# Kernel tuning notes

Hardware: AMD Instinct MI355X
Metric: run time of the kernel (lower is better)

The kernel has to match this reference:

```python
import jax, jax.numpy as jnp
import numpy as np

N_ITER = 5
B = 16            # graphs
NPG = 3125        # nodes per graph
EPG = 50000       # edges per graph
N_NODES = B * NPG # 50000
E = B * EPG       # 800000
F = 32            # f_e = f_x = f_u
H = 64            # hidden


def _lin(key, fan_in, fan_out):
    k1, k2 = jax.random.split(key)
    s = 1.0 / np.sqrt(fan_in)
    W = jax.random.uniform(k1, (fan_in, fan_out), jnp.float32, -s, s)
    b = jax.random.uniform(k2, (fan_out,), jnp.float32, -s, s)
    return W, b


def setup_inputs() -> dict:
    key = jax.random.key(0)
    ks = jax.random.split(key, 12)
    x = jax.random.normal(ks[0], (N_NODES, F), jnp.float32)
    edge_attr = jax.random.normal(ks[1], (E, F), jnp.float32)
    y = jax.random.normal(ks[2], (B, F), jnp.float32)
    # within-graph random edges: graph g owns nodes [g*NPG, (g+1)*NPG)
    off = (jnp.arange(B, dtype=jnp.int32) * NPG)[:, None]          # [B,1]
    src = jax.random.randint(ks[3], (B, EPG), 0, NPG, jnp.int32) + off
    dst = jax.random.randint(ks[4], (B, EPG), 0, NPG, jnp.int32) + off
    edge_index = jnp.stack([src.reshape(-1), dst.reshape(-1)])      # [2,E]
    batch = jnp.repeat(jnp.arange(B, dtype=jnp.int32), NPG)         # [N]
    # shared GN-block parameters (one block reused for all N_ITER steps)
    We1, be1 = _lin(ks[5], F + 2 * F + F, H)   # edge MLP: [src,dst,e,u[b]]
    We2, be2 = _lin(ks[6], H, F)
    Wn1, bn1 = _lin(ks[7], F + F + F, H)       # node MLP: [x,e_agg,u[b]]
    Wn2, bn2 = _lin(ks[8], H, F)
    Wg1, bg1 = _lin(ks[9], F + F + F, H)       # global MLP: [x_agg,e_agg,u]
    Wg2, bg2 = _lin(ks[10], H, F)
    return dict(x=x, edge_attr=edge_attr, y=y,
                We1=We1, be1=be1, We2=We2, be2=be2,
                Wn1=Wn1, bn1=bn1, Wn2=Wn2, bn2=bn2,
                Wg1=Wg1, bg1=bg1, Wg2=Wg2, bg2=bg2,
                edge_index=edge_index, batch=batch)


def _mlp(h_in, W1, b1, W2, b2):
    return jax.nn.relu(h_in @ W1 + b1) @ W2 + b2


def _segment_mean(vals, seg, num):
    s = jax.ops.segment_sum(vals, seg, num_segments=num)
    c = jax.ops.segment_sum(jnp.ones((vals.shape[0], 1), vals.dtype), seg,
                            num_segments=num)
    return s / jnp.maximum(c, 1.0)


def _gn_forward(x, edge_attr, y, params, edge_index, batch):
    (We1, be1, We2, be2, Wn1, bn1, Wn2, bn2, Wg1, bg1, Wg2, bg2) = params
    row, col = edge_index[0], edge_index[1]
    e_batch = batch[row]
    for _ in range(N_ITER):  # shared-weight unrolled GN block
        # EdgeModel: phi_e([src, dest, e, u[batch_e]])
        e_in = jnp.concatenate([x[row], x[col], edge_attr, y[e_batch]], axis=1)
        edge_attr = _mlp(e_in, We1, be1, We2, be2)
        # NodeModel: mean of incoming edges (scatter over col)
        e_agg_node = _segment_mean(edge_attr, col, N_NODES)
        n_in = jnp.concatenate([x, e_agg_node, y[batch]], axis=1)
        x = _mlp(n_in, Wn1, bn1, Wn2, bn2)
        # GlobalModel: per-graph means of edges and nodes
        e_agg = _segment_mean(edge_attr, e_batch, B)
        x_agg = _segment_mean(x, batch, B)
        g_in = jnp.concatenate([x_agg, e_agg, y], axis=1)
        y = _mlp(g_in, Wg1, bg1, Wg2, bg2)
    return x, edge_attr, y


def reference(x, edge_attr, y,
              We1, be1, We2, be2,
              Wn1, bn1, Wn2, bn2,
              Wg1, bg1, Wg2, bg2,
              edge_index, batch):
    params = (We1, be1, We2, be2, Wn1, bn1, Wn2, bn2, Wg1, bg1, Wg2, bg2)
    return _gn_forward(x, edge_attr, y, params, edge_index, batch)
```

## Files before the change

kernel.cpp:

```cpp
#include <hip/hip_runtime.h>

#define NITER   5
#define B_G     16
#define NPG     3125
#define EPG     50000
#define NNODES  50000
#define NEDGES  800000
#define FD      32
#define HD      64

#define EDGE_TPG   391
#define EDGE_BLOCKS 1024

#define NODE_TPG   25
#define NODE_BLOCKS (B_G * NODE_TPG)

typedef __attribute__((ext_vector_type(4))) float f32x4;
typedef __attribute__((ext_vector_type(8))) short bf16x8;
typedef __attribute__((ext_vector_type(4))) unsigned int u32x4;

union FragU { bf16x8 v; unsigned int u[4]; u32x4 q; };

__device__ __forceinline__ void fsplit2(float a, float b,
                                        unsigned int& hi, unsigned int& lo) {
    unsigned int ua = __float_as_uint(a), ub = __float_as_uint(b);
    float la = a - __uint_as_float(ua & 0xffff0000u);
    float lb = b - __uint_as_float(ub & 0xffff0000u);
    hi = __builtin_amdgcn_perm(ub, ua, 0x07060302u);
    lo = __builtin_amdgcn_perm(__float_as_uint(lb), __float_as_uint(la), 0x07060302u);
}
__device__ __forceinline__ unsigned int fpack_hl(float v) {
    unsigned int uv = __float_as_uint(v);
    float lv = v - __uint_as_float(uv & 0xffff0000u);
    return __builtin_amdgcn_perm(__float_as_uint(lv), uv, 0x07060302u);
}
__device__ __forceinline__ bf16x8 ldfrag(const unsigned int* p) {
    FragU t; t.q = *(const u32x4*)p; return t.v;
}

__global__ __launch_bounds__(1024) void wsplit_kernel(
    const float* __restrict__ We1, const float* __restrict__ We2,
    const float* __restrict__ Wn1, const float* __restrict__ Wn2,
    unsigned int* __restrict__ wsp)
{
    for (int item = threadIdx.x; item < 1792; item += 1024) {
        const float* W; unsigned int* dst; int lda, s, n, l;
        if (item < 768)       { int f = item >> 6;          l = item & 63; s = f >> 2; n = f & 3; W = We1; lda = 64; dst = wsp + f * 512; }
        else if (item < 1024) { int f = (item - 768) >> 6;  l = item & 63; s = f >> 1; n = f & 1; W = We2; lda = 32; dst = wsp + 6144 + f * 512; }
        else if (item < 1536) { int f = (item - 1024) >> 6; l = item & 63; s = f >> 2; n = f & 3; W = Wn1; lda = 64; dst = wsp + 8192 + f * 512; }
        else                  { int f = (item - 1536) >> 6; l = item & 63; s = f >> 1; n = f & 1; W = Wn2; lda = 32; dst = wsp + 12288 + f * 512; }
        int lm = l & 15, lg = l >> 4;
        int rowbase = s * 32 + lg * 8;
        int col = n * 16 + lm;
        #pragma unroll
        for (int p = 0; p < 4; ++p) {
            float a = W[(rowbase + 2 * p) * lda + col];
            float b = W[(rowbase + 2 * p + 1) * lda + col];
            unsigned int hi, lo;
            fsplit2(a, b, hi, lo);
            dst[l * 4 + p] = hi;
            dst[256 + l * 4 + p] = lo;
        }
    }
}


__global__ __launch_bounds__(256) void count_kernel(const int* __restrict__ coli,
                                                    int* __restrict__ cnt)
{
    int e = blockIdx.x * 256 + threadIdx.x;
    if (e < NEDGES) atomicAdd(&cnt[coli[e]], 1);
}

__global__ __launch_bounds__(1024) void scan_blocks_kernel(const int* __restrict__ deg,
                                                           int* __restrict__ off,
                                                           int* __restrict__ bsum, int n)
{
    __shared__ int buf[1024];
    int tid = threadIdx.x;
    int idx = blockIdx.x * 1024 + tid;
    int v = (idx < n) ? deg[idx] : 0;
    buf[tid] = v;
    __syncthreads();
    for (int o = 1; o < 1024; o <<= 1) {
        int t = (tid >= o) ? buf[tid - o] : 0;
        __syncthreads();
        buf[tid] += t;
        __syncthreads();
    }
    if (idx < n) off[idx] = buf[tid] - v;
    if (tid == 1023) bsum[blockIdx.x] = buf[1023];
}

__global__ __launch_bounds__(64) void scan_carry_kernel(int* __restrict__ bsum,
                                                        int* __restrict__ off,
                                                        int nb, int n)
{
    if (threadIdx.x == 0) {
        int c = 0;
        for (int i = 0; i < nb; ++i) { int t = bsum[i]; bsum[i] = c; c += t; }
        off[n] = c;
    }
}

__global__ __launch_bounds__(1024) void scan_add_kernel(const int* __restrict__ bsum,
                                                        int* __restrict__ off, int n)
{
    int idx = blockIdx.x * 1024 + threadIdx.x;
    if (idx < n) off[idx] += bsum[blockIdx.x];
}

__global__ __launch_bounds__(256) void fill_kernel(const int* __restrict__ coli,
                                                   const int* __restrict__ off,
                                                   int* __restrict__ cursor,
                                                   int* __restrict__ csr)
{
    int e = blockIdx.x * 256 + threadIdx.x;
    if (e < NEDGES) {
        int c = coli[e];
        int pos = atomicAdd(&cursor[c], 1);
        csr[off[c] + pos] = e;
    }
}


__global__ __launch_bounds__(1024) void prep_kernel(
    const float* __restrict__ y,
    const float* __restrict__ We1, const float* __restrict__ be1,
    const float* __restrict__ Wn1, const float* __restrict__ bn1,
    float* __restrict__ cu_e, float* __restrict__ cu_n,
    float* __restrict__ xagg, float* __restrict__ eagg)
{
    int tid = threadIdx.x;
    if (tid < B_G * FD) xagg[tid] = 0.0f;
    else                eagg[tid - B_G * FD] = 0.0f;

    int g = tid >> 6;
    int j = tid & 63;
    float ae = be1[j];
    float an = bn1[j];
    for (int k = 0; k < FD; ++k) {
        float yv = y[g * FD + k];
        ae = fmaf(yv, We1[(96 + k) * HD + j], ae);
        an = fmaf(yv, Wn1[(64 + k) * HD + j], an);
    }
    cu_e[g * HD + j] = ae;
    cu_n[g * HD + j] = an;
}

__global__ __launch_bounds__(256) void edge_mfma_kernel(
    const float* __restrict__ x,
    const float* __restrict__ ea_in,
    const int* __restrict__ rowi,
    const int* __restrict__ coli,
    const unsigned int* __restrict__ wsp,
    const float* __restrict__ be2,
    const float* __restrict__ cu_e,
    float* __restrict__ ea_out,
    float* __restrict__ eagg)
{
    __shared__ unsigned int h_lds[4][32][68];

    const int tid = threadIdx.x;
    const int wid = tid >> 6;
    const int l   = tid & 63;
    const int lm  = l & 15;
    const int lg  = l >> 4;
    const int koff = lg * 8;

    bf16x8 w1h[3][4], w1l[3][4];
    #pragma unroll
    for (int s = 0; s < 3; ++s)
        #pragma unroll
        for (int n = 0; n < 4; ++n) {
            const unsigned int* p = wsp + (s * 4 + n) * 512 + l * 4;
            w1h[s][n] = ldfrag(p);
            w1l[s][n] = ldfrag(p + 256);
        }
    bf16x8 w2h[2][2], w2l[2][2];
    #pragma unroll
    for (int s = 0; s < 2; ++s)
        #pragma unroll
        for (int n = 0; n < 2; ++n) {
            const unsigned int* p = wsp + 6144 + (s * 2 + n) * 512 + l * 4;
            w2h[s][n] = ldfrag(p);
            w2l[s][n] = ldfrag(p + 256);
        }
    float bias2[2];
    bias2[0] = be2[lm];
    bias2[1] = be2[16 + lm];

    const int b   = blockIdx.x;
    const int xcd = b & 7;
    const int i   = b >> 3;
    const int g   = 2 * xcd + (i >> 6);
    const int j0  = i & 63;
    const long gbase = (long)g * EPG;
    const long gend  = gbase + EPG;

    float bcu[4];
    #pragma unroll
    for (int n = 0; n < 4; ++n) bcu[n] = cu_e[g * HD + n * 16 + lm];

    int nidx[2], nrr[2], ncc[2];
    #pragma unroll
    for (int t = 0; t < 2; ++t) {
        long e = gbase + (long)j0 * 128 + wid * 32 + t * 16 + lm;
        if (e >= gend) e = gend - 1;
        nidx[t] = (int)e;
        nrr[t] = rowi[nidx[t]];
        ncc[t] = coli[nidx[t]];
    }

    for (int lt = j0; lt < EDGE_TPG; lt += 64) {
        int eidx[2], rr[2], cc[2];
        #pragma unroll
        for (int t = 0; t < 2; ++t) { eidx[t] = nidx[t]; rr[t] = nrr[t]; cc[t] = ncc[t]; }

        int nlt = lt + 64;
        if (nlt < EDGE_TPG) {
            #pragma unroll
            for (int t = 0; t < 2; ++t) {
                long e = gbase + (long)nlt * 128 + wid * 32 + t * 16 + lm;
                if (e >= gend) e = gend - 1;
                nidx[t] = (int)e;
                nrr[t] = rowi[nidx[t]];
                ncc[t] = coli[nidx[t]];
            }
        }

        const long e0 = gbase + (long)lt * 128 + wid * 32;

        f32x4 va[2][3][2];
        #pragma unroll
        for (int t = 0; t < 2; ++t) {
            const float* p0 = x     + (long)rr[t]   * FD + koff;
            const float* p1 = x     + (long)cc[t]   * FD + koff;
            const float* p2 = ea_in + (long)eidx[t] * FD + koff;
            va[t][0][0] = *(const f32x4*)p0; va[t][0][1] = *(const f32x4*)(p0 + 4);
            va[t][1][0] = *(const f32x4*)p1; va[t][1][1] = *(const f32x4*)(p1 + 4);
            va[t][2][0] = *(const f32x4*)p2; va[t][2][1] = *(const f32x4*)(p2 + 4);
        }

        f32x4 acc1[2][4];
        #pragma unroll
        for (int n = 0; n < 4; ++n) {
            #pragma unroll
            for (int t = 0; t < 2; ++t) acc1[t][n] = (f32x4){bcu[n], bcu[n], bcu[n], bcu[n]};
        }

        #pragma unroll
        for (int t = 0; t < 2; ++t) {
            #pragma unroll
            for (int s = 0; s < 3; ++s) {
                FragU ah, al;
                #pragma unroll
                for (int q = 0; q < 2; ++q)
                    #pragma unroll
                    for (int p = 0; p < 2; ++p)
                        fsplit2(va[t][s][q][2 * p], va[t][s][q][2 * p + 1],
                                ah.u[q * 2 + p], al.u[q * 2 + p]);
                #pragma unroll
                for (int n = 0; n < 4; ++n) {
                    acc1[t][n] = __builtin_amdgcn_mfma_f32_16x16x32_bf16(ah.v, w1h[s][n], acc1[t][n], 0, 0, 0);
                    acc1[t][n] = __builtin_amdgcn_mfma_f32_16x16x32_bf16(ah.v, w1l[s][n], acc1[t][n], 0, 0, 0);
                    acc1[t][n] = __builtin_amdgcn_mfma_f32_16x16x32_bf16(al.v, w1h[s][n], acc1[t][n], 0, 0, 0);
                }
            }
        }

        #pragma unroll
        for (int t = 0; t < 2; ++t)
            #pragma unroll
            for (int n = 0; n < 4; ++n)
                #pragma unroll
                for (int r = 0; r < 4; ++r)
                    h_lds[wid][t * 16 + lg * 4 + r][n * 16 + lm] =
                        fpack_hl(fmaxf(acc1[t][n][r], 0.0f));
        asm volatile("s_waitcnt lgkmcnt(0)" ::: "memory");
        __builtin_amdgcn_sched_barrier(0);

        f32x4 acc2[2][2];
        #pragma unroll
        for (int n = 0; n < 2; ++n) {
            #pragma unroll
            for (int t = 0; t < 2; ++t) acc2[t][n] = (f32x4){bias2[n], bias2[n], bias2[n], bias2[n]};
        }
        #pragma unroll
        for (int t = 0; t < 2; ++t) {
            #pragma unroll
            for (int s = 0; s < 2; ++s) {
                const unsigned int* hp = &h_lds[wid][t * 16 + lm][s * 32 + koff];
                unsigned int u0 = hp[0], u1 = hp[1], u2 = hp[2], u3 = hp[3];
                unsigned int u4 = hp[4], u5 = hp[5], u6 = hp[6], u7 = hp[7];
                FragU ah, al;
                ah.u[0] = __builtin_amdgcn_perm(u1, u0, 0x05040100u);
                ah.u[1] = __builtin_amdgcn_perm(u3, u2, 0x05040100u);
                ah.u[2] = __builtin_amdgcn_perm(u5, u4, 0x05040100u);
                ah.u[3] = __builtin_amdgcn_perm(u7, u6, 0x05040100u);
                al.u[0] = __builtin_amdgcn_perm(u1, u0, 0x07060302u);
                al.u[1] = __builtin_amdgcn_perm(u3, u2, 0x07060302u);
                al.u[2] = __builtin_amdgcn_perm(u5, u4, 0x07060302u);
                al.u[3] = __builtin_amdgcn_perm(u7, u6, 0x07060302u);
                #pragma unroll
                for (int n = 0; n < 2; ++n) {
                    acc2[t][n] = __builtin_amdgcn_mfma_f32_16x16x32_bf16(ah.v, w2h[s][n], acc2[t][n], 0, 0, 0);
                    acc2[t][n] = __builtin_amdgcn_mfma_f32_16x16x32_bf16(ah.v, w2l[s][n], acc2[t][n], 0, 0, 0);
                    acc2[t][n] = __builtin_amdgcn_mfma_f32_16x16x32_bf16(al.v, w2h[s][n], acc2[t][n], 0, 0, 0);
                }
            }
        }

        #pragma unroll
        for (int t = 0; t < 2; ++t)
            #pragma unroll
            for (int r = 0; r < 4; ++r) {
                long e = e0 + t * 16 + lg * 4 + r;
                if (e < gend) {
                    ea_out[e * FD + lm]      = acc2[t][0][r];
                    ea_out[e * FD + 16 + lm] = acc2[t][1][r];
                }
            }

        #pragma unroll
        for (int n = 0; n < 2; ++n) {
            float s = 0.0f;
            #pragma unroll
            for (int t = 0; t < 2; ++t)
                #pragma unroll
                for (int r = 0; r < 4; ++r) {
                    long e = e0 + t * 16 + lg * 4 + r;
                    s += (e < gend) ? acc2[t][n][r] : 0.0f;
                }
            s += __shfl_xor(s, 16, 64);
            s += __shfl_xor(s, 32, 64);
            if (lg == 0) atomicAdd(&eagg[g * FD + n * 16 + lm], s);
        }
    }
}

__global__ __launch_bounds__(256) void agg_kernel(
    const float* __restrict__ ea,
    const int* __restrict__ off,
    const int* __restrict__ csr,
    float* __restrict__ e_mean)
{
    int wid = threadIdx.x >> 6;
    int l   = threadIdx.x & 63;
    int slot = l >> 5;
    int f    = l & 31;
    int n = blockIdx.x * 4 + wid;
    int s0 = off[n], s1 = off[n + 1];
    float acc = 0.0f;
    for (int i = s0 + slot; i < s1; i += 2) {
        int eid = csr[i];
        acc += ea[(long)eid * FD + f];
    }
    acc += __shfl_xor(acc, 32, 64);
    int deg = s1 - s0;
    float inv = 1.0f / (float)(deg > 1 ? deg : 1);
    if (l < 32) e_mean[(long)n * FD + f] = acc * inv;
}

__global__ __launch_bounds__(256) void node_mfma_kernel(
    const float* __restrict__ x_in,
    const float* __restrict__ e_mean,
    const unsigned int* __restrict__ wsp,
    const float* __restrict__ bn2,
    const float* __restrict__ cu_n,
    float* __restrict__ x_out,
    float* __restrict__ xagg)
{
    __shared__ unsigned int h_lds[4][32][68];

    const int tid = threadIdx.x;
    const int wid = tid >> 6;
    const int l   = tid & 63;
    const int lm  = l & 15;
    const int lg  = l >> 4;
    const int koff = lg * 8;

    bf16x8 w1h[2][4], w1l[2][4];
    #pragma unroll
    for (int s = 0; s < 2; ++s)
        #pragma unroll
        for (int n = 0; n < 4; ++n) {
            const unsigned int* p = wsp + (s * 4 + n) * 512 + l * 4;
            w1h[s][n] = ldfrag(p);
            w1l[s][n] = ldfrag(p + 256);
        }
    bf16x8 w2h[2][2], w2l[2][2];
    #pragma unroll
    for (int s = 0; s < 2; ++s)
        #pragma unroll
        for (int n = 0; n < 2; ++n) {
            const unsigned int* p = wsp + 4096 + (s * 2 + n) * 512 + l * 4;
            w2h[s][n] = ldfrag(p);
            w2l[s][n] = ldfrag(p + 256);
        }
    float bias2[2];
    bias2[0] = bn2[lm];
    bias2[1] = bn2[16 + lm];

    const int g  = blockIdx.x / NODE_TPG;
    const int lt = blockIdx.x - g * NODE_TPG;
    const int nb = lt * 128 + wid * 32;

    f32x4 va[2][2][2];
    #pragma unroll
    for (int t = 0; t < 2; ++t) {
        int rl = nb + t * 16 + lm;
        if (rl > NPG - 1) rl = NPG - 1;
        long node = (long)g * NPG + rl;
        const float* p0 = x_in   + node * FD + koff;
        const float* p1 = e_mean + node * FD + koff;
        va[t][0][0] = *(const f32x4*)p0; va[t][0][1] = *(const f32x4*)(p0 + 4);
        va[t][1][0] = *(const f32x4*)p1; va[t][1][1] = *(const f32x4*)(p1 + 4);
    }

    f32x4 acc1[2][4];
    #pragma unroll
    for (int n = 0; n < 4; ++n) {
        float b = cu_n[g * HD + n * 16 + lm];
        #pragma unroll
        for (int t = 0; t < 2; ++t) acc1[t][n] = (f32x4){b, b, b, b};
    }

    #pragma unroll
    for (int t = 0; t < 2; ++t) {
        #pragma unroll
        for (int s = 0; s < 2; ++s) {
            FragU ah, al;
            #pragma unroll
            for (int q = 0; q < 2; ++q)
                #pragma unroll
                for (int p = 0; p < 2; ++p)
                    fsplit2(va[t][s][q][2 * p], va[t][s][q][2 * p + 1],
                            ah.u[q * 2 + p], al.u[q * 2 + p]);
            #pragma unroll
            for (int n = 0; n < 4; ++n) {
                acc1[t][n] = __builtin_amdgcn_mfma_f32_16x16x32_bf16(ah.v, w1h[s][n], acc1[t][n], 0, 0, 0);
                acc1[t][n] = __builtin_amdgcn_mfma_f32_16x16x32_bf16(ah.v, w1l[s][n], acc1[t][n], 0, 0, 0);
                acc1[t][n] = __builtin_amdgcn_mfma_f32_16x16x32_bf16(al.v, w1h[s][n], acc1[t][n], 0, 0, 0);
            }
        }
    }

    #pragma unroll
    for (int t = 0; t < 2; ++t)
        #pragma unroll
        for (int n = 0; n < 4; ++n)
            #pragma unroll
            for (int r = 0; r < 4; ++r)
                h_lds[wid][t * 16 + lg * 4 + r][n * 16 + lm] =
                    fpack_hl(fmaxf(acc1[t][n][r], 0.0f));
    asm volatile("s_waitcnt lgkmcnt(0)" ::: "memory");
    __builtin_amdgcn_sched_barrier(0);

    f32x4 acc2[2][2];
    #pragma unroll
    for (int n = 0; n < 2; ++n) {
        #pragma unroll
        for (int t = 0; t < 2; ++t) acc2[t][n] = (f32x4){bias2[n], bias2[n], bias2[n], bias2[n]};
    }
    #pragma unroll
    for (int t = 0; t < 2; ++t) {
        #pragma unroll
        for (int s = 0; s < 2; ++s) {
            const unsigned int* hp = &h_lds[wid][t * 16 + lm][s * 32 + koff];
            unsigned int u0 = hp[0], u1 = hp[1], u2 = hp[2], u3 = hp[3];
            unsigned int u4 = hp[4], u5 = hp[5], u6 = hp[6], u7 = hp[7];
            FragU ah, al;
            ah.u[0] = __builtin_amdgcn_perm(u1, u0, 0x05040100u);
            ah.u[1] = __builtin_amdgcn_perm(u3, u2, 0x05040100u);
            ah.u[2] = __builtin_amdgcn_perm(u5, u4, 0x05040100u);
            ah.u[3] = __builtin_amdgcn_perm(u7, u6, 0x05040100u);
            al.u[0] = __builtin_amdgcn_perm(u1, u0, 0x07060302u);
            al.u[1] = __builtin_amdgcn_perm(u3, u2, 0x07060302u);
            al.u[2] = __builtin_amdgcn_perm(u5, u4, 0x07060302u);
            al.u[3] = __builtin_amdgcn_perm(u7, u6, 0x07060302u);
            #pragma unroll
            for (int n = 0; n < 2; ++n) {
                acc2[t][n] = __builtin_amdgcn_mfma_f32_16x16x32_bf16(ah.v, w2h[s][n], acc2[t][n], 0, 0, 0);
                acc2[t][n] = __builtin_amdgcn_mfma_f32_16x16x32_bf16(ah.v, w2l[s][n], acc2[t][n], 0, 0, 0);
                acc2[t][n] = __builtin_amdgcn_mfma_f32_16x16x32_bf16(al.v, w2h[s][n], acc2[t][n], 0, 0, 0);
            }
        }
    }

    #pragma unroll
    for (int t = 0; t < 2; ++t)
        #pragma unroll
        for (int r = 0; r < 4; ++r) {
            int rl = nb + t * 16 + lg * 4 + r;
            if (rl < NPG) {
                long node = (long)g * NPG + rl;
                x_out[node * FD + lm]      = acc2[t][0][r];
                x_out[node * FD + 16 + lm] = acc2[t][1][r];
            }
        }

    #pragma unroll
    for (int n = 0; n < 2; ++n) {
        float s = 0.0f;
        #pragma unroll
        for (int t = 0; t < 2; ++t)
            #pragma unroll
            for (int r = 0; r < 4; ++r) {
                int rl = nb + t * 16 + lg * 4 + r;
                s += (rl < NPG) ? acc2[t][n][r] : 0.0f;
            }
        s += __shfl_xor(s, 16, 64);
        s += __shfl_xor(s, 32, 64);
        if (lg == 0) atomicAdd(&xagg[g * FD + n * 16 + lm], s);
    }
}

__global__ __launch_bounds__(1024) void global_kernel(
    const float* __restrict__ y_in,
    float* __restrict__ xagg, float* __restrict__ eagg,
    const float* __restrict__ Wg1, const float* __restrict__ bg1,
    const float* __restrict__ Wg2, const float* __restrict__ bg2,
    const float* __restrict__ We1, const float* __restrict__ be1,
    const float* __restrict__ Wn1, const float* __restrict__ bn1,
    float* __restrict__ y_out,
    float* __restrict__ cu_e, float* __restrict__ cu_n)
{
    __shared__ float in_lds[B_G][100];
    __shared__ float h_lds2[B_G][HD + 1];
    __shared__ float y_lds[B_G][FD];
    int tid = threadIdx.x;
    for (int idx = tid; idx < B_G * 96; idx += 1024) {
        int g2 = idx / 96, k = idx % 96;
        float v;
        if (k < 32)      v = xagg[g2 * 32 + k] * (1.0f / NPG);
        else if (k < 64) v = eagg[g2 * 32 + (k - 32)] * (1.0f / EPG);
        else             v = y_in[g2 * 32 + (k - 64)];
        in_lds[g2][k] = v;
    }
    __syncthreads();
    int g = tid >> 6, j = tid & 63;
    float h = bg1[j];
    for (int k = 0; k < 96; ++k)
        h = fmaf(in_lds[g][k], Wg1[k * HD + j], h);
    h_lds2[g][j] = fmaxf(h, 0.0f);
    __syncthreads();
    if (j < FD) {
        float o = bg2[j];
        for (int k = 0; k < HD; ++k)
            o = fmaf(h_lds2[g][k], Wg2[k * FD + j], o);
        y_out[g * FD + j] = o;
        y_lds[g][j] = o;
    }
    __syncthreads();
    float ae = be1[j];
    float an = bn1[j];
    for (int k = 0; k < FD; ++k) {
        float yv = y_lds[g][k];
        ae = fmaf(yv, We1[(96 + k) * HD + j], ae);
        an = fmaf(yv, Wn1[(64 + k) * HD + j], an);
    }
    cu_e[g * HD + j] = ae;
    cu_n[g * HD + j] = an;
    if (tid < B_G * FD)            xagg[tid] = 0.0f;
    else if (tid < 2 * B_G * FD)   eagg[tid - B_G * FD] = 0.0f;
}


extern "C" void kernel_launch(void* const* d_in, const int* in_sizes, int n_in,
                              void* d_out, int out_size, void* d_ws, size_t ws_size,
                              hipStream_t stream)
{
    const float* x0  = (const float*)d_in[0];
    const float* ea0 = (const float*)d_in[1];
    const float* y0  = (const float*)d_in[2];
    const float* We1 = (const float*)d_in[3];
    const float* be1 = (const float*)d_in[4];
    const float* We2 = (const float*)d_in[5];
    const float* be2 = (const float*)d_in[6];
    const float* Wn1 = (const float*)d_in[7];
    const float* bn1 = (const float*)d_in[8];
    const float* Wn2 = (const float*)d_in[9];
    const float* bn2 = (const float*)d_in[10];
    const float* Wg1 = (const float*)d_in[11];
    const float* bg1 = (const float*)d_in[12];
    const float* Wg2 = (const float*)d_in[13];
    const float* bg2 = (const float*)d_in[14];
    const int*   ei  = (const int*)d_in[15];
    const int* rowi = ei;
    const int* coli = ei + NEDGES;

    float* out_x  = (float*)d_out;
    float* out_ea = out_x + (size_t)NNODES * FD;
    float* out_y  = out_ea + (size_t)NEDGES * FD;

    char* ws = (char*)d_ws;
    int*   off    = (int*)(ws + 0);
    int*   cursor = (int*)(ws + 200192);
    int*   csr    = (int*)(ws + 400384);
    float* xagg   = (float*)(ws + 3600384);
    float* eagg   = xagg + B_G * FD;
    float* cu_e   = (float*)(ws + 3604480);
    float* cu_n   = cu_e + B_G * HD;
    float* e_mean = (float*)(ws + 3612672);
    unsigned int* wsp  = (unsigned int*)(ws + 10012672);
    int*   bsum   = (int*)(ws + 10070016);

    wsplit_kernel<<<1, 1024, 0, stream>>>(We1, We2, Wn1, Wn2, wsp);
    hipMemsetAsync(cursor, 0, NNODES * sizeof(int), stream);
    count_kernel<<<(NEDGES + 255) / 256, 256, 0, stream>>>(coli, cursor);
    scan_blocks_kernel<<<49, 1024, 0, stream>>>(cursor, off, bsum, NNODES);
    scan_carry_kernel<<<1, 64, 0, stream>>>(bsum, off, 49, NNODES);
    scan_add_kernel<<<49, 1024, 0, stream>>>(bsum, off, NNODES);
    hipMemsetAsync(cursor, 0, NNODES * sizeof(int), stream);
    fill_kernel<<<(NEDGES + 255) / 256, 256, 0, stream>>>(coli, off, cursor, csr);

    prep_kernel<<<1, 1024, 0, stream>>>(y0, We1, be1, Wn1, bn1,
                                        cu_e, cu_n, xagg, eagg);

    for (int it = 0; it < NITER; ++it) {
        const float* xc  = (it == 0) ? x0  : out_x;
        const float* eac = (it == 0) ? ea0 : out_ea;
        const float* yc  = (it == 0) ? y0  : out_y;

        edge_mfma_kernel<<<EDGE_BLOCKS, 256, 0, stream>>>(xc, eac, rowi, coli,
                                                          wsp, be2, cu_e,
                                                          out_ea, eagg);
        agg_kernel<<<NNODES / 4, 256, 0, stream>>>(out_ea, off, csr, e_mean);
        node_mfma_kernel<<<NODE_BLOCKS, 256, 0, stream>>>(xc, e_mean,
                                                          wsp + 8192, bn2, cu_n,
                                                          out_x, xagg);
        global_kernel<<<1, 1024, 0, stream>>>(yc, xagg, eagg,
                                              Wg1, bg1, Wg2, bg2,
                                              We1, be1, Wn1, bn1,
                                              out_y, cu_e, cu_n);
    }
}
```

Before: 742.7 us.

## Pre-split node features to bf16 hi/lo and double-buffer edge gathers

Adds a per-iteration kernel that converts node features into packed bf16 hi/lo pairs once, so the edge kernel gathers pre-split fragments instead of splitting each gathered row per edge. The edge loop is restructured into a two-stage software pipeline: it prefetches indices two tiles ahead and node fragments one tile ahead while the current tile computes. The aggregation kernel now loads CSR indices with one wave-wide load and shuffles them out, then reads float4 vectors per lane and reduces across lanes with shuffles. The extra kernel launch, its added traffic, and higher register pressure from the double buffering are the costs.

```diff
diff --git a/kernel.cpp b/kernel.cpp
--- a/kernel.cpp
+++ b/kernel.cpp
@@ -62,6 +62,24 @@
             dst[256 + l * 4 + p] = lo;
         }
     }
+}
+
+__global__ __launch_bounds__(256) void xsplit_kernel(
+    const float* __restrict__ xin, unsigned int* __restrict__ x_sp)
+{
+    int t = blockIdx.x * 256 + threadIdx.x;
+    if (t >= NNODES * 4) return;
+    int n = t >> 2, c = t & 3;
+    long base = (long)n * 32 + c * 8;
+    f32x4 a = *(const f32x4*)(xin + base);
+    f32x4 b = *(const f32x4*)(xin + base + 4);
+    unsigned int h[4], lo[4];
+    fsplit2(a[0], a[1], h[0], lo[0]);
+    fsplit2(a[2], a[3], h[1], lo[1]);
+    fsplit2(b[0], b[1], h[2], lo[2]);
+    fsplit2(b[2], b[3], h[3], lo[3]);
+    *(u32x4*)(x_sp + (long)n * 32 + c * 4)      = (u32x4){h[0], h[1], h[2], h[3]};
+    *(u32x4*)(x_sp + (long)n * 32 + 16 + c * 4) = (u32x4){lo[0], lo[1], lo[2], lo[3]};
 }
 
 
@@ -149,7 +167,7 @@
 }
 
 __global__ __launch_bounds__(256) void edge_mfma_kernel(
-    const float* __restrict__ x,
+    const unsigned int* __restrict__ x_sp,
     const float* __restrict__ ea_in,
     const int* __restrict__ rowi,
     const int* __restrict__ coli,
@@ -202,70 +220,76 @@
     #pragma unroll
     for (int n = 0; n < 4; ++n) bcu[n] = cu_e[g * HD + n * 16 + lm];
 
-    int nidx[2], nrr[2], ncc[2];
-    #pragma unroll
-    for (int t = 0; t < 2; ++t) {
-        long e = gbase + (long)j0 * 128 + wid * 32 + t * 16 + lm;
-        if (e >= gend) e = gend - 1;
-        nidx[t] = (int)e;
-        nrr[t] = rowi[nidx[t]];
-        ncc[t] = coli[nidx[t]];
-    }
-
-    for (int lt = j0; lt < EDGE_TPG; lt += 64) {
-        int eidx[2], rr[2], cc[2];
-        #pragma unroll
-        for (int t = 0; t < 2; ++t) { eidx[t] = nidx[t]; rr[t] = nrr[t]; cc[t] = ncc[t]; }
-
-        int nlt = lt + 64;
-        if (nlt < EDGE_TPG) {
-            #pragma unroll
-            for (int t = 0; t < 2; ++t) {
-                long e = gbase + (long)nlt * 128 + wid * 32 + t * 16 + lm;
-                if (e >= gend) e = gend - 1;
-                nidx[t] = (int)e;
-                nrr[t] = rowi[nidx[t]];
-                ncc[t] = coli[nidx[t]];
-            }
-        }
-
+    auto idx_load = [&](int (&rr)[2], int (&cc)[2], int lt) {
+        #pragma unroll
+        for (int t = 0; t < 2; ++t) {
+            long e = gbase + (long)lt * 128 + wid * 32 + t * 16 + lm;
+            if (e >= gend) e = gend - 1;
+            rr[t] = rowi[e];
+            cc[t] = coli[e];
+        }
+    };
+    auto x_load = [&](u32x4 (&xh)[2][2], u32x4 (&xl)[2][2],
+                      const int (&rr)[2], const int (&cc)[2]) {
+        #pragma unroll
+        for (int t = 0; t < 2; ++t) {
+            const unsigned int* pr = x_sp + (long)rr[t] * 32;
+            const unsigned int* pc = x_sp + (long)cc[t] * 32;
+            xh[t][0] = *(const u32x4*)(pr + lg * 4);
+            xl[t][0] = *(const u32x4*)(pr + 16 + lg * 4);
+            xh[t][1] = *(const u32x4*)(pc + lg * 4);
+            xl[t][1] = *(const u32x4*)(pc + 16 + lg * 4);
+        }
+    };
+
+    auto compute = [&](int lt, u32x4 (&xh)[2][2], u32x4 (&xl)[2][2]) {
         const long e0 = gbase + (long)lt * 128 + wid * 32;
 
-        f32x4 va[2][3][2];
+        f32x4 vea[2][2];
         #pragma unroll
         for (int t = 0; t < 2; ++t) {
-            const float* p0 = x     + (long)rr[t]   * FD + koff;
-            const float* p1 = x     + (long)cc[t]   * FD + koff;
-            const float* p2 = ea_in + (long)eidx[t] * FD + koff;
-            va[t][0][0] = *(const f32x4*)p0; va[t][0][1] = *(const f32x4*)(p0 + 4);
-            va[t][1][0] = *(const f32x4*)p1; va[t][1][1] = *(const f32x4*)(p1 + 4);
-            va[t][2][0] = *(const f32x4*)p2; va[t][2][1] = *(const f32x4*)(p2 + 4);
+            long e = e0 + t * 16 + lm;
+            if (e >= gend) e = gend - 1;
+            const float* p2 = ea_in + e * FD + koff;
+            vea[t][0] = *(const f32x4*)p2;
+            vea[t][1] = *(const f32x4*)(p2 + 4);
         }
 
         f32x4 acc1[2][4];
         #pragma unroll
-        for (int n = 0; n < 4; ++n) {
-            #pragma unroll
-            for (int t = 0; t < 2; ++t) acc1[t][n] = (f32x4){bcu[n], bcu[n], bcu[n], bcu[n]};
-        }
-
-        #pragma unroll
-        for (int t = 0; t < 2; ++t) {
-            #pragma unroll
-            for (int s = 0; s < 3; ++s) {
+        for (int n = 0; n < 4; ++n)
+            #pragma unroll
+            for (int t = 0; t < 2; ++t)
+                acc1[t][n] = (f32x4){bcu[n], bcu[n], bcu[n], bcu[n]};
+
+        #pragma unroll
+        for (int t = 0; t < 2; ++t)
+            #pragma unroll
+            for (int s = 0; s < 2; ++s) {
                 FragU ah, al;
-                #pragma unroll
-                for (int q = 0; q < 2; ++q)
-                    #pragma unroll
-                    for (int p = 0; p < 2; ++p)
-                        fsplit2(va[t][s][q][2 * p], va[t][s][q][2 * p + 1],
-                                ah.u[q * 2 + p], al.u[q * 2 + p]);
+                ah.q = xh[t][s];
+                al.q = xl[t][s];
                 #pragma unroll
                 for (int n = 0; n < 4; ++n) {
                     acc1[t][n] = __builtin_amdgcn_mfma_f32_16x16x32_bf16(ah.v, w1h[s][n], acc1[t][n], 0, 0, 0);
                     acc1[t][n] = __builtin_amdgcn_mfma_f32_16x16x32_bf16(ah.v, w1l[s][n], acc1[t][n], 0, 0, 0);
                     acc1[t][n] = __builtin_amdgcn_mfma_f32_16x16x32_bf16(al.v, w1h[s][n], acc1[t][n], 0, 0, 0);
                 }
+            }
+        #pragma unroll
+        for (int t = 0; t < 2; ++t) {
+            FragU ah, al;
+            #pragma unroll
+            for (int q = 0; q < 2; ++q)
+                #pragma unroll
+                for (int p = 0; p < 2; ++p)
+                    fsplit2(vea[t][q][2 * p], vea[t][q][2 * p + 1],
+                            ah.u[q * 2 + p], al.u[q * 2 + p]);
+            #pragma unroll
+            for (int n = 0; n < 4; ++n) {
+                acc1[t][n] = __builtin_amdgcn_mfma_f32_16x16x32_bf16(ah.v, w1h[2][n], acc1[t][n], 0, 0, 0);
+                acc1[t][n] = __builtin_amdgcn_mfma_f32_16x16x32_bf16(ah.v, w1l[2][n], acc1[t][n], 0, 0, 0);
+                acc1[t][n] = __builtin_amdgcn_mfma_f32_16x16x32_bf16(al.v, w1h[2][n], acc1[t][n], 0, 0, 0);
             }
         }
 
@@ -282,12 +306,12 @@
 
         f32x4 acc2[2][2];
         #pragma unroll
-        for (int n = 0; n < 2; ++n) {
-            #pragma unroll
-            for (int t = 0; t < 2; ++t) acc2[t][n] = (f32x4){bias2[n], bias2[n], bias2[n], bias2[n]};
-        }
-        #pragma unroll
-        for (int t = 0; t < 2; ++t) {
+        for (int n = 0; n < 2; ++n)
+            #pragma unroll
+            for (int t = 0; t < 2; ++t)
+                acc2[t][n] = (f32x4){bias2[n], bias2[n], bias2[n], bias2[n]};
+        #pragma unroll
+        for (int t = 0; t < 2; ++t)
             #pragma unroll
             for (int s = 0; s < 2; ++s) {
                 const unsigned int* hp = &h_lds[wid][t * 16 + lm][s * 32 + koff];
@@ -309,7 +333,6 @@
                     acc2[t][n] = __builtin_amdgcn_mfma_f32_16x16x32_bf16(al.v, w2h[s][n], acc2[t][n], 0, 0, 0);
                 }
             }
-        }
 
         #pragma unroll
         for (int t = 0; t < 2; ++t)
@@ -336,6 +359,27 @@
             s += __shfl_xor(s, 32, 64);
             if (lg == 0) atomicAdd(&eagg[g * FD + n * 16 + lm], s);
         }
+    };
+
+    int rrA[2], ccA[2], rrB[2], ccB[2];
+    u32x4 xhA[2][2], xlA[2][2], xhB[2][2], xlB[2][2];
+
+    idx_load(rrA, ccA, j0);
+    x_load(xhA, xlA, rrA, ccA);
+    idx_load(rrB, ccB, j0 + 64);
+
+    auto step = [&](int lt,
+                    u32x4 (&xh)[2][2], u32x4 (&xl)[2][2], int (&rrD)[2], int (&ccD)[2],
+                    u32x4 (&xhN)[2][2], u32x4 (&xlN)[2][2], int (&rrN)[2], int (&ccN)[2]) {
+        idx_load(rrD, ccD, lt + 128);
+        x_load(xhN, xlN, rrN, ccN);
+        compute(lt, xh, xl);
+    };
+
+    for (int lt = j0; lt < EDGE_TPG; lt += 128) {
+        step(lt, xhA, xlA, rrA, ccA, xhB, xlB, rrB, ccB);
+        if (lt + 64 < EDGE_TPG)
+            step(lt + 64, xhB, xlB, rrB, ccB, xhA, xlA, rrA, ccA);
     }
 }
 
@@ -347,19 +391,47 @@
 {
     int wid = threadIdx.x >> 6;
     int l   = threadIdx.x & 63;
-    int slot = l >> 5;
-    int f    = l & 31;
+    int rq  = l >> 3;
+    int q   = l & 7;
     int n = blockIdx.x * 4 + wid;
     int s0 = off[n], s1 = off[n + 1];
-    float acc = 0.0f;
-    for (int i = s0 + slot; i < s1; i += 2) {
-        int eid = csr[i];
-        acc += ea[(long)eid * FD + f];
-    }
-    acc += __shfl_xor(acc, 32, 64);
     int deg = s1 - s0;
+
+    f32x4 acc = {0.0f, 0.0f, 0.0f, 0.0f};
+    if (deg > 0) {
+        int cl = (l < deg) ? l : 0;
+        int cidx = csr[s0 + cl];
+        #pragma unroll
+        for (int r = 0; r < 8; ++r) {
+            int src = r * 8 + rq;
+            int eid = __shfl(cidx, src, 64);
+            if (src < deg) {
+                f32x4 v = *(const f32x4*)(ea + (long)eid * FD + q * 4);
+                acc += v;
+            }
+        }
+        if (deg > 64) {
+            for (int i = s0 + 64; i < s1; i += 8) {
+                int ii = i + rq;
+                if (ii < s1) {
+                    int eid = csr[ii];
+                    acc += *(const f32x4*)(ea + (long)eid * FD + q * 4);
+                }
+            }
+        }
+    }
+    #pragma unroll
+    for (int m = 8; m < 64; m <<= 1) {
+        acc[0] += __shfl_xor(acc[0], m, 64);
+        acc[1] += __shfl_xor(acc[1], m, 64);
+        acc[2] += __shfl_xor(acc[2], m, 64);
+        acc[3] += __shfl_xor(acc[3], m, 64);
+    }
     float inv = 1.0f / (float)(deg > 1 ? deg : 1);
-    if (l < 32) e_mean[(long)n * FD + f] = acc * inv;
+    if (l < 8) {
+        f32x4 o = {acc[0] * inv, acc[1] * inv, acc[2] * inv, acc[3] * inv};
+        *(f32x4*)(e_mean + (long)n * FD + q * 4) = o;
+    }
 }
 
 __global__ __launch_bounds__(256) void node_mfma_kernel(
@@ -603,8 +675,9 @@
     float* cu_e   = (float*)(ws + 3604480);
     float* cu_n   = cu_e + B_G * HD;
     float* e_mean = (float*)(ws + 3612672);
-    unsigned int* wsp  = (unsigned int*)(ws + 10012672);
+    unsigned int* wsp = (unsigned int*)(ws + 10012672);
     int*   bsum   = (int*)(ws + 10070016);
+    unsigned int* x_sp = (unsigned int*)(ws + 10070272);
 
     wsplit_kernel<<<1, 1024, 0, stream>>>(We1, We2, Wn1, Wn2, wsp);
     hipMemsetAsync(cursor, 0, NNODES * sizeof(int), stream);
@@ -623,7 +696,8 @@
         const float* eac = (it == 0) ? ea0 : out_ea;
         const float* yc  = (it == 0) ? y0  : out_y;
 
-        edge_mfma_kernel<<<EDGE_BLOCKS, 256, 0, stream>>>(xc, eac, rowi, coli,
+        xsplit_kernel<<<(NNODES * 4 + 255) / 256, 256, 0, stream>>>(xc, x_sp);
+        edge_mfma_kernel<<<EDGE_BLOCKS, 256, 0, stream>>>(x_sp, eac, rowi, coli,
                                                           wsp, be2, cu_e,
                                                           out_ea, eagg);
         agg_kernel<<<NNODES / 4, 256, 0, stream>>>(out_ea, off, csr, e_mean);
```

Result: faster. 667.2 us (-10.2%).
